# Kernel tuning notes

Measured on AMD Instinct MI355X. Metric: run time of the kernel, lower is better.

The kernel has to match this reference:

```python
import jax, jax.numpy as jnp
import numpy as np

V, D, L, H, T_BLK, DFF = 50257, 768, 12, 12, 1024, 4096
DK = D // H
LN_EPS = 1e-5


def setup_inputs() -> dict:
    key = jax.random.key(0)
    ks = jax.random.split(key, 16)
    s = 0.02
    inp = {
        "idx": jax.random.randint(ks[0], (2, 1024), 0, V),
        "tok_emb": jax.random.normal(ks[1], (V, D), jnp.float32) * s,
        "pos_emb": jax.random.normal(ks[2], (1, T_BLK, D), jnp.float32) * s,
        "ln1_w": jnp.ones((L, D), jnp.float32),
        "ln1_b": jnp.zeros((L, D), jnp.float32),
        "qkv_w": jax.random.normal(ks[3], (L, 3 * D, D), jnp.float32) * s,
        "qkv_b": jnp.zeros((L, 3 * D), jnp.float32),
        "proj_w": jax.random.normal(ks[4], (L, D, D), jnp.float32) * s,
        "proj_b": jnp.zeros((L, D), jnp.float32),
        "ln2_w": jnp.ones((L, D), jnp.float32),
        "ln2_b": jnp.zeros((L, D), jnp.float32),
        "ff1_w": jax.random.normal(ks[5], (L, DFF, D), jnp.float32) * s,
        "ff1_b": jnp.zeros((L, DFF), jnp.float32),
        "ff2_w": jax.random.normal(ks[6], (L, D, DFF), jnp.float32) * s,
        "ff2_b": jnp.zeros((L, D), jnp.float32),
        "lnf_w": jnp.ones((D,), jnp.float32),
        "lnf_b": jnp.zeros((D,), jnp.float32),
        "head_w": jax.random.normal(ks[7], (V, D), jnp.float32) * s,
    }
    return inp


def _layernorm(x, w, b):
    mu = jnp.mean(x, axis=-1, keepdims=True)
    var = jnp.var(x, axis=-1, keepdims=True)
    return (x - mu) * jax.lax.rsqrt(var + LN_EPS) * w + b


def _gpt_forward(idx, tok_emb, pos_emb, ln1_w, ln1_b, qkv_w, qkv_b, proj_w, proj_b,
                 ln2_w, ln2_b, ff1_w, ff1_b, ff2_w, ff2_b, lnf_w, lnf_b, head_w):
    B, T = idx.shape
    x = tok_emb[idx] + pos_emb[:, :T, :]  # [B,T,D]
    mask = jnp.tril(jnp.ones((T, T), bool))  # causal
    scale = 1.0 / np.sqrt(DK)

    def step(x, p):
        l1w, l1b, qw, qb, pw, pb, l2w, l2b, f1w, f1b, f2w, f2b = p
        h = _layernorm(x, l1w, l1b)
        qkv = h @ qw.T + qb  # [B,T,3D]
        q, k, v = jnp.split(qkv, 3, axis=-1)
        q = q.reshape(B, T, H, DK).transpose(0, 2, 1, 3)  # [B,H,T,DK]
        k = k.reshape(B, T, H, DK).transpose(0, 2, 1, 3)
        v = v.reshape(B, T, H, DK).transpose(0, 2, 1, 3)
        att = jnp.einsum('bhtd,bhsd->bhts', q, k) * scale
        att = jnp.where(mask, att, -jnp.inf)
        att = jax.nn.softmax(att, axis=-1)
        y = jnp.einsum('bhts,bhsd->bhtd', att, v)
        y = y.transpose(0, 2, 1, 3).reshape(B, T, D)
        x = x + y @ pw.T + pb
        h2 = _layernorm(x, l2w, l2b)
        ff = jax.nn.gelu(h2 @ f1w.T + f1b, approximate=False) @ f2w.T + f2b
        return x + ff, None

    params = (ln1_w, ln1_b, qkv_w, qkv_b, proj_w, proj_b,
              ln2_w, ln2_b, ff1_w, ff1_b, ff2_w, ff2_b)
    x, _ = jax.lax.scan(step, x, params)
    x = _layernorm(x, lnf_w, lnf_b)
    return x @ head_w.T  # [B,T,V] logits


def reference(idx, tok_emb, pos_emb, ln1_w, ln1_b, qkv_w, qkv_b, proj_w, proj_b,
              ln2_w, ln2_b, ff1_w, ff1_b, ff2_w, ff2_b, lnf_w, lnf_b, head_w):
    return _gpt_forward(idx, tok_emb, pos_emb, ln1_w, ln1_b, qkv_w, qkv_b, proj_w,
                        proj_b, ln2_w, ln2_b, ff1_w, ff1_b, ff2_w, ff2_b,
                        lnf_w, lnf_b, head_w)
```

## Files before the change

### kernel.cpp

```cpp
#include <hip/hip_runtime.h>
#include <hip/hip_bf16.h>
#include <math.h>

#define Dm 768
#define Tt 1024
#define Bb 2
#define Hh 12
#define DFF 4096
#define Ll 12
#define Vv 50257
#define ROWS (Bb*Tt)
#define LN_EPS 1e-5f

typedef unsigned int uint;
typedef unsigned short ushort;
typedef float f32x4 __attribute__((ext_vector_type(4)));
typedef short bf16x8 __attribute__((ext_vector_type(8)));
typedef ushort us8 __attribute__((ext_vector_type(8)));

__device__ __forceinline__ ushort f2bf(float f) {
  uint u = __builtin_bit_cast(uint, f);
  u += 0x7FFFu + ((u >> 16) & 1u);
  return (ushort)(u >> 16);
}

#define GLL(gp, lp)                                                          \
  __builtin_amdgcn_global_load_lds(                                          \
      (const __attribute__((address_space(1))) uint*)(gp),                   \
      (__attribute__((address_space(3))) uint*)(lp), 16, 0, 0)

__global__ __launch_bounds__(256) void embed_ln(
    const int* __restrict__ idx, const float* __restrict__ tok,
    const float* __restrict__ pos, const float* __restrict__ w,
    const float* __restrict__ b, float* __restrict__ x,
    ushort* __restrict__ out) {
  const int row = blockIdx.x;
  const int t = row & (Tt - 1);
  const int tid = threadIdx.x;
  const float* tsrc = tok + (size_t)idx[row] * Dm;
  const float* psrc = pos + (size_t)t * Dm;
  float v[3];
  float sum = 0.f, sq = 0.f;
#pragma unroll
  for (int i = 0; i < 3; i++) {
    const int d = tid + i * 256;
    v[i] = tsrc[d] + psrc[d];
    x[(size_t)row * Dm + d] = v[i];
    sum += v[i]; sq += v[i] * v[i];
  }
#pragma unroll
  for (int off = 32; off > 0; off >>= 1) {
    sum += __shfl_xor(sum, off);
    sq  += __shfl_xor(sq, off);
  }
  __shared__ float red[8];
  const int wid = tid >> 6, lane = tid & 63;
  if (lane == 0) { red[wid] = sum; red[wid + 4] = sq; }
  __syncthreads();
  sum = red[0] + red[1] + red[2] + red[3];
  sq  = red[4] + red[5] + red[6] + red[7];
  const float mu = sum * (1.f / Dm);
  const float var = sq * (1.f / Dm) - mu * mu;
  const float rstd = rsqrtf(var + LN_EPS);
  ushort* dst = out + (size_t)row * Dm;
#pragma unroll
  for (int i = 0; i < 3; i++) {
    const int d = tid + i * 256;
    dst[d] = f2bf((v[i] - mu) * rstd * w[d] + b[d]);
  }
}

__global__ __launch_bounds__(256) void red_ln(
    const float* __restrict__ part, int nsk, const float* __restrict__ bias,
    float* __restrict__ x, const float* __restrict__ w,
    const float* __restrict__ b, ushort* __restrict__ out) {
  const int row = blockIdx.x;
  const int tid = threadIdx.x;
  float v[3];
  float sum = 0.f, sq = 0.f;
#pragma unroll
  for (int i = 0; i < 3; i++) {
    const int d = tid + i * 256;
    const size_t off = (size_t)row * Dm + d;
    float s = x[off] + bias[d];
    for (int k = 0; k < nsk; k++) s += part[(size_t)k * ROWS * Dm + off];
    x[off] = s;
    v[i] = s;
    sum += s; sq += s * s;
  }
#pragma unroll
  for (int off = 32; off > 0; off >>= 1) {
    sum += __shfl_xor(sum, off);
    sq  += __shfl_xor(sq, off);
  }
  __shared__ float red[8];
  const int wid = tid >> 6, lane = tid & 63;
  if (lane == 0) { red[wid] = sum; red[wid + 4] = sq; }
  __syncthreads();
  sum = red[0] + red[1] + red[2] + red[3];
  sq  = red[4] + red[5] + red[6] + red[7];
  const float mu = sum * (1.f / Dm);
  const float var = sq * (1.f / Dm) - mu * mu;
  const float rstd = rsqrtf(var + LN_EPS);
  ushort* dst = out + (size_t)row * Dm;
#pragma unroll
  for (int i = 0; i < 3; i++) {
    const int d = tid + i * 256;
    dst[d] = f2bf((v[i] - mu) * rstd * w[d] + b[d]);
  }
}

__global__ __launch_bounds__(256) void convert_w(
    const float* __restrict__ s, ushort* __restrict__ d, int n4) {
  const int stride = gridDim.x * 256;
  for (int i = blockIdx.x * 256 + threadIdx.x; i < n4; i += stride) {
    const float4 v = ((const float4*)s)[i];
    ushort4 o;
    o.x = f2bf(v.x); o.y = f2bf(v.y); o.z = f2bf(v.z); o.w = f2bf(v.w);
    ((ushort4*)d)[i] = o;
  }
}

#define EPI_QKV 0
#define EPI_PART 1
#define EPI_BIAS_GELU 2
#define EPI_NONE 3

template <int EPI>
__global__ __launch_bounds__(256) void gemm_mfma(
    const ushort* __restrict__ A, const ushort* __restrict__ B,
    const float* __restrict__ bias, void* __restrict__ Cv,
    void* __restrict__ Cv2, int Kloop, int Kstr, int Nloc, int ldC) {
  __shared__ char lds[32768];
  const int tid = threadIdx.x;
  const int l = tid & 63;
  const int wid = __builtin_amdgcn_readfirstlane(tid >> 6);
  const int wr = wid >> 1, wc = wid & 1;
  const int m0 = blockIdx.y * 128;
  const int n0 = blockIdx.x * 128;
  const int z = (EPI == EPI_PART) ? blockIdx.z : 0;
  if (EPI == EPI_PART) { A += (size_t)z * Kloop; B += (size_t)z * Kloop; }

  const int cperm = (((l & 3) ^ ((l >> 3) & 3)) * 8);
  const ushort* gA = A + (size_t)(m0 + wid * 32 + (l >> 2)) * Kstr + cperm;
  int rB = n0 + wid * 32 + (l >> 2);
  rB = min(rB, Nloc - 1);
  const ushort* gB = B + (size_t)rB * Kstr + cperm;

  const int rdSw = (l & 15) * 64 + (((l >> 4) ^ ((l >> 1) & 3)) * 16);
  const int aRd = wr * 4096 + rdSw;
  const int bRd = 8192 + wc * 4096 + rdSw;

  f32x4 acc[4][4] = {};
  const int nt = Kloop / 32;

  {
    const int lb = wid * 2048;
    GLL(gA, lds + lb);          GLL(gA + 16 * Kstr, lds + lb + 1024);
    GLL(gB, lds + 8192 + lb);   GLL(gB + 16 * Kstr, lds + 8192 + lb + 1024);
  }

  for (int t = 0; t < nt; ++t) {
    __syncthreads();
    if (t + 1 < nt) {
      const int base = ((t + 1) & 1) * 16384;
      const int lb = base + wid * 2048;
      const ushort* a = gA + (t + 1) * 32;
      const ushort* b = gB + (t + 1) * 32;
      GLL(a, lds + lb);         GLL(a + 16 * Kstr, lds + lb + 1024);
      GLL(b, lds + 8192 + lb);  GLL(b + 16 * Kstr, lds + 8192 + lb + 1024);
    }
    const int base = (t & 1) * 16384;
    bf16x8 av[4], bv[4];
#pragma unroll
    for (int i = 0; i < 4; ++i) {
      av[i] = *(const bf16x8*)(lds + base + aRd + i * 1024);
      bv[i] = *(const bf16x8*)(lds + base + bRd + i * 1024);
    }
#pragma unroll
    for (int i = 0; i < 4; ++i)
#pragma unroll
      for (int j = 0; j < 4; ++j)
        acc[i][j] = __builtin_amdgcn_mfma_f32_16x16x32_bf16(
            av[i], bv[j], acc[i][j], 0, 0, 0);
  }

#pragma unroll
  for (int fm = 0; fm < 4; ++fm) {
    const int row0 = m0 + wr * 64 + fm * 16 + (l >> 4) * 4;
#pragma unroll
    for (int fn = 0; fn < 4; ++fn) {
      const int col = n0 + wc * 64 + fn * 16 + (l & 15);
      if (col >= Nloc) continue;
      float bi = 0.f;
      if (EPI == EPI_QKV || EPI == EPI_BIAS_GELU) bi = bias[col];
      if (EPI == EPI_QKV && col >= 2 * Dm) {
        const int hh = (col - 2 * Dm) >> 6, dd = col & 63;
        const int bI = row0 >> 10, t0 = row0 & (Tt - 1);
        ushort4 o4;
        o4.x = f2bf(acc[fm][fn][0] + bi);
        o4.y = f2bf(acc[fm][fn][1] + bi);
        o4.z = f2bf(acc[fm][fn][2] + bi);
        o4.w = f2bf(acc[fm][fn][3] + bi);
        *(ushort4*)((ushort*)Cv2 +
                    ((size_t)((bI * Hh + hh) * 64 + dd)) * Tt + t0) = o4;
        continue;
      }
#pragma unroll
      for (int r = 0; r < 4; ++r) {
        float v = acc[fm][fn][r] + bi;
        const size_t off = (size_t)(row0 + r) * ldC + col;
        if (EPI == EPI_BIAS_GELU) {
          v = 0.5f * v * (1.f + erff(v * 0.70710678118654752f));
          ((ushort*)Cv)[off] = f2bf(v);
        } else if (EPI == EPI_QKV) {
          ((ushort*)Cv)[off] = f2bf(v);
        } else if (EPI == EPI_PART) {
          ((float*)Cv)[(size_t)z * ROWS * ldC + off] = v;
        } else {
          ((float*)Cv)[off] = v;
        }
      }
    }
  }
}

__global__ __launch_bounds__(128) void attn_mfma(
    const ushort* __restrict__ qkv, const ushort* __restrict__ vTg,
    ushort* __restrict__ y) {
  __shared__ char lds[36864];
  const int tid = threadIdx.x;
  const int l = tid & 63;
  const int w = tid >> 6;
  const int s = l & 15, g = l >> 4;
  const int bq = blockIdx.x, h = blockIdx.y, b = blockIdx.z;
  const int bh = b * Hh + h;

  const int qrow = bq * 32 + w * 16 + s;
  const ushort* qp = qkv + (size_t)(b * Tt + qrow) * 2304 + h * 64 + g * 8;
  const bf16x8 aq0 = *(const bf16x8*)qp;
  const bf16x8 aq1 = *(const bf16x8*)(qp + 32);

  size_t gofs[8];
#pragma unroll
  for (int i = 0; i < 8; i++) {
    const int c = tid + i * 128;
    if (i < 4) {
      const int kr = c >> 3;
      gofs[i] = (size_t)(b * Tt + kr) * 2304 + Dm + h * 64 + ((c & 7) ^ (kr & 7)) * 8;
    } else {
      const int cv = c - 512;
      const int vr = cv >> 3;
      gofs[i] = (size_t)(bh * 64 + vr) * Tt + ((cv & 7) ^ (vr & 7)) * 8;
    }
  }

#define ASTAGE(kt, base)                                                     \
  do {                                                                       \
    _Pragma("unroll")                                                        \
    for (int i = 0; i < 8; i++) {                                            \
      const ushort* p = (i < 4) ? (qkv + gofs[i] + (size_t)(kt) * 147456)    \
                                : (vTg + gofs[i] + (kt) * 64);               \
      GLL(p, lds + (base) + tid * 16 + i * 2048);                            \
    }                                                                        \
  } while (0)

  f32x4 oc[4] = {};
  float mrun[4], lrun[4];
#pragma unroll
  for (int r = 0; r < 4; r++) { mrun[r] = -INFINITY; lrun[r] = 0.f; }

  const int pB = 32768 + w * 2048;
  const int kSw = (s & 7);
  const int nkt = (bq >> 1) + 1;

  ASTAGE(0, 0);
  for (int kt = 0; kt < nkt; ++kt) {
    __syncthreads();
    if (kt + 1 < nkt) ASTAGE(kt + 1, ((kt + 1) & 1) * 16384);
    const int cur = (kt & 1) * 16384;

    f32x4 sc[4];
#pragma unroll
    for (int jn = 0; jn < 4; jn++) {
      const int krow = cur + (jn * 16 + s) * 128;
      const bf16x8 bk0 = *(const bf16x8*)(lds + krow + ((g ^ kSw) * 16));
      const bf16x8 bk1 = *(const bf16x8*)(lds + krow + (((4 + g) ^ kSw) * 16));
      f32x4 z = {};
      z = __builtin_amdgcn_mfma_f32_16x16x32_bf16(aq0, bk0, z, 0, 0, 0);
      z = __builtin_amdgcn_mfma_f32_16x16x32_bf16(aq1, bk1, z, 0, 0, 0);
      sc[jn] = z;
    }

    float cr[4];
    const bool diag = (kt == nkt - 1);
#pragma unroll
    for (int r = 0; r < 4; r++) {
      const int rowg = bq * 32 + w * 16 + g * 4 + r;
      float v[4];
#pragma unroll
      for (int jn = 0; jn < 4; jn++) {
        v[jn] = sc[jn][r] * 0.125f;
        if (diag && (kt * 64 + jn * 16 + s) > rowg) v[jn] = -INFINITY;
      }
      float mx = fmaxf(fmaxf(v[0], v[1]), fmaxf(v[2], v[3]));
      mx = fmaxf(mx, __shfl_xor(mx, 1));
      mx = fmaxf(mx, __shfl_xor(mx, 2));
      mx = fmaxf(mx, __shfl_xor(mx, 4));
      mx = fmaxf(mx, __shfl_xor(mx, 8));
      const float mnew = fmaxf(mrun[r], mx);
      const float corr = __expf(mrun[r] - mnew);
      mrun[r] = mnew;
      float ps = 0.f;
#pragma unroll
      for (int jn = 0; jn < 4; jn++) {
        const float p = __expf(v[jn] - mnew);
        ps += p;
        *(ushort*)(lds + pB + (g * 4 + r) * 128 +
                   (((2 * jn + (s >> 3)) ^ g) * 16) + (s & 7) * 2) = f2bf(p);
      }
      ps += __shfl_xor(ps, 1);
      ps += __shfl_xor(ps, 2);
      ps += __shfl_xor(ps, 4);
      ps += __shfl_xor(ps, 8);
      lrun[r] = lrun[r] * corr + ps;
      cr[r] = corr;
    }

    const float c01 = (s & 1) ? cr[1] : cr[0];
    const float c23 = (s & 1) ? cr[3] : cr[2];
    const float csel = (s & 2) ? c23 : c01;
    const float ccol = __shfl(csel, ((s >> 2) << 4) | s);
#pragma unroll
    for (int fm = 0; fm < 4; fm++) {
      oc[fm][0] *= ccol; oc[fm][1] *= ccol;
      oc[fm][2] *= ccol; oc[fm][3] *= ccol;
    }

    const bf16x8 bp0 = *(const bf16x8*)(lds + pB + s * 128 + ((g ^ (s >> 2)) * 16));
    const bf16x8 bp1 = *(const bf16x8*)(lds + pB + s * 128 + (((4 + g) ^ (s >> 2)) * 16));
#pragma unroll
    for (int fm = 0; fm < 4; fm++) {
      const int vrow = cur + 8192 + (fm * 16 + s) * 128;
      const bf16x8 av0 = *(const bf16x8*)(lds + vrow + ((g ^ kSw) * 16));
      const bf16x8 av1 = *(const bf16x8*)(lds + vrow + (((4 + g) ^ kSw) * 16));
      oc[fm] = __builtin_amdgcn_mfma_f32_16x16x32_bf16(av0, bp0, oc[fm], 0, 0, 0);
      oc[fm] = __builtin_amdgcn_mfma_f32_16x16x32_bf16(av1, bp1, oc[fm], 0, 0, 0);
    }
  }

  float li[4];
#pragma unroll
  for (int r = 0; r < 4; r++) li[r] = 1.f / lrun[r];
  const float l01 = (s & 1) ? li[1] : li[0];
  const float l23 = (s & 1) ? li[3] : li[2];
  const float lsel = (s & 2) ? l23 : l01;
  const float lcol = __shfl(lsel, ((s >> 2) << 4) | s);
  ushort* yp = y + (size_t)(b * Tt + qrow) * Dm + h * 64;
#pragma unroll
  for (int fm = 0; fm < 4; fm++) {
    ushort4 o4;
    o4.x = f2bf(oc[fm][0] * lcol);
    o4.y = f2bf(oc[fm][1] * lcol);
    o4.z = f2bf(oc[fm][2] * lcol);
    o4.w = f2bf(oc[fm][3] * lcol);
    *(ushort4*)(yp + fm * 16 + g * 4) = o4;
  }
}

extern "C" void kernel_launch(void* const* d_in, const int* in_sizes, int n_in,
                              void* d_out, int out_size, void* d_ws, size_t ws_size,
                              hipStream_t stream) {
  const int* idx = (const int*)d_in[0];
  const float* tok = (const float*)d_in[1];
  const float* pos = (const float*)d_in[2];
  const float* ln1w = (const float*)d_in[3];
  const float* ln1b = (const float*)d_in[4];
  const float* qkvw = (const float*)d_in[5];
  const float* qkvb = (const float*)d_in[6];
  const float* projw = (const float*)d_in[7];
  const float* projb = (const float*)d_in[8];
  const float* ln2w = (const float*)d_in[9];
  const float* ln2b = (const float*)d_in[10];
  const float* ff1w = (const float*)d_in[11];
  const float* ff1b = (const float*)d_in[12];
  const float* ff2w = (const float*)d_in[13];
  const float* ff2b = (const float*)d_in[14];
  const float* lnfw = (const float*)d_in[15];
  const float* lnfb = (const float*)d_in[16];
  const float* headw = (const float*)d_in[17];
  float* out = (float*)d_out;

  char* ws = (char*)d_ws;
  ushort* h    = (ushort*)ws;
  float*  x    = (float*)(ws + 3145728);
  ushort* y    = (ushort*)(ws + 9437184);
  ushort* qkv  = (ushort*)(ws + 12582912);
  ushort* vTg  = (ushort*)(ws + 22020096);
  ushort* ff   = (ushort*)(ws + 25165824);
  ushort* wb   = (ushort*)(ws + 41943040);
  float* projPart = (float*)(ws + 12582912);
  float* ff2Part  = (float*)(ws + 9437184);

  const size_t oPROJ = (size_t)Ll * 3 * Dm * Dm;
  const size_t oFF1  = oPROJ + (size_t)Ll * Dm * Dm;
  const size_t oFF2  = oFF1 + (size_t)Ll * DFF * Dm;
  const size_t oHEAD = oFF2 + (size_t)Ll * Dm * DFF;

  convert_w<<<2048, 256, 0, stream>>>(qkvw, wb, (int)(oPROJ / 4));
  convert_w<<<2048, 256, 0, stream>>>(projw, wb + oPROJ, (int)((oFF1 - oPROJ) / 4));
  convert_w<<<2048, 256, 0, stream>>>(ff1w, wb + oFF1, (int)((oFF2 - oFF1) / 4));
  convert_w<<<2048, 256, 0, stream>>>(ff2w, wb + oFF2, (int)((oHEAD - oFF2) / 4));
  convert_w<<<2048, 256, 0, stream>>>(headw, wb + oHEAD, (int)((size_t)Vv * Dm / 4));

  embed_ln<<<ROWS, 256, 0, stream>>>(idx, tok, pos, ln1w, ln1b, x, h);

  for (int l = 0; l < Ll; l++) {
    gemm_mfma<EPI_QKV><<<dim3(18, 16), 256, 0, stream>>>(
        h, wb + (size_t)l * 3 * Dm * Dm, qkvb + l * 3 * Dm, qkv, vTg,
        Dm, Dm, 3 * Dm, 3 * Dm);
    attn_mfma<<<dim3(32, Hh, Bb), 128, 0, stream>>>(qkv, vTg, y);
    gemm_mfma<EPI_PART><<<dim3(6, 16, 2), 256, 0, stream>>>(
        y, wb + oPROJ + (size_t)l * Dm * Dm, nullptr, projPart, nullptr,
        Dm / 2, Dm, Dm, Dm);
    red_ln<<<ROWS, 256, 0, stream>>>(projPart, 2, projb + l * Dm, x,
                                     ln2w + l * Dm, ln2b + l * Dm, h);
    gemm_mfma<EPI_BIAS_GELU><<<dim3(32, 16), 256, 0, stream>>>(
        h, wb + oFF1 + (size_t)l * DFF * Dm, ff1b + l * DFF, ff, nullptr,
        Dm, Dm, DFF, DFF);
    gemm_mfma<EPI_PART><<<dim3(6, 16, 2), 256, 0, stream>>>(
        ff, wb + oFF2 + (size_t)l * Dm * DFF, nullptr, ff2Part, nullptr,
        DFF / 2, DFF, Dm, Dm);
    const float* nw = (l == Ll - 1) ? lnfw : ln1w + (l + 1) * Dm;
    const float* nb = (l == Ll - 1) ? lnfb : ln1b + (l + 1) * Dm;
    red_ln<<<ROWS, 256, 0, stream>>>(ff2Part, 2, ff2b + l * Dm, x, nw, nb, h);
  }

  gemm_mfma<EPI_NONE><<<dim3(393, 16), 256, 0, stream>>>(
      h, wb + oHEAD, nullptr, out, nullptr, Dm, Dm, Vv, Vv);
}
```

Baseline: 2.245 ms.

## Add dedicated 256x256-tile LM-head GEMM with 4-stage pipeline; raise MFMA priority in attention

Replaces the generic GEMM used for the vocabulary projection with a specialized kernel using 256x256 output tiles, 8 waves, a 4-buffer async global-to-LDS pipeline over K=768, a swizzled block ordering for L2 reuse, and s_setprio around MFMA bursts. The larger tile is meant to raise arithmetic intensity and reduce operand refetch on the largest GEMM in the forward pass. It also wraps the attention MFMA loops with s_setprio. The tile uses 128KB of LDS and many accumulators, which risks low occupancy, and the ragged last vocab panel relies on clamped loads.

New measurement: 2.225 ms. About the same (-0.9%).

```diff
diff --git a/kernel.cpp b/kernel.cpp
--- a/kernel.cpp
+++ b/kernel.cpp
@@ -225,6 +225,106 @@
   }
 }
 
+__global__ __launch_bounds__(512, 2) void gemm_head8(
+    const ushort* __restrict__ A, const ushort* __restrict__ B,
+    float* __restrict__ C) {
+  __shared__ char lds[131072];
+  const int tid = threadIdx.x;
+  const int l = tid & 63;
+  const int wid = __builtin_amdgcn_readfirstlane(tid >> 6);
+  const int wm = wid >> 2, wn = wid & 3;
+
+  const int bid = blockIdx.x;
+  const int swz = (bid & 7) * 197 + (bid >> 3);
+  const int pan = swz >> 3, mrw = swz & 7;
+  const int m0 = mrw * 256;
+  const int n0 = pan * 256;
+
+  const ushort* gA[2];
+  const ushort* gB[2];
+#pragma unroll
+  for (int j = 0; j < 2; j++) {
+    const int c = tid + j * 512;
+    const int r = c >> 2, kq = c & 3;
+    gA[j] = A + (size_t)(m0 + r) * Dm + ((kq ^ (r & 3)) * 8);
+    int rb = n0 + r;
+    rb = min(rb, Vv - 1);
+    gB[j] = B + (size_t)rb * Dm + ((kq ^ (r & 3)) * 8);
+  }
+
+#define HSTAGE(t)                                                            \
+  do {                                                                       \
+    char* _lb = lds + ((t) & 3) * 32768;                                     \
+    const int _o = (t) * 32;                                                 \
+    GLL(gA[0] + _o, _lb + tid * 16);                                         \
+    GLL(gA[1] + _o, _lb + 8192 + tid * 16);                                  \
+    GLL(gB[0] + _o, _lb + 16384 + tid * 16);                                 \
+    GLL(gB[1] + _o, _lb + 24576 + tid * 16);                                 \
+  } while (0)
+
+  f32x4 acc[8][4] = {};
+  const int s = l & 15, g = l >> 4;
+
+  int aOff[8], bOff[4];
+#pragma unroll
+  for (int fm = 0; fm < 8; fm++) {
+    const int r = wm * 128 + fm * 16 + s;
+    aOff[fm] = r * 64 + ((g ^ (r & 3)) * 16);
+  }
+#pragma unroll
+  for (int fn = 0; fn < 4; fn++) {
+    const int r = wn * 64 + fn * 16 + s;
+    bOff[fn] = 16384 + r * 64 + ((g ^ (r & 3)) * 16);
+  }
+
+  HSTAGE(0); HSTAGE(1); HSTAGE(2);
+  asm volatile("s_waitcnt vmcnt(8)" ::: "memory");
+  __builtin_amdgcn_s_barrier();
+  __builtin_amdgcn_sched_barrier(0);
+
+#define HITER(t, VC)                                                         \
+  {                                                                          \
+    if ((t) + 3 < 24) HSTAGE((t) + 3);                                       \
+    char* bb = lds + ((t) & 3) * 32768;                                      \
+    bf16x8 av[8], bv[4];                                                     \
+    _Pragma("unroll")                                                        \
+    for (int fm = 0; fm < 8; fm++) av[fm] = *(const bf16x8*)(bb + aOff[fm]); \
+    _Pragma("unroll")                                                        \
+    for (int fn = 0; fn < 4; fn++) bv[fn] = *(const bf16x8*)(bb + bOff[fn]); \
+    __builtin_amdgcn_s_setprio(1);                                           \
+    _Pragma("unroll")                                                        \
+    for (int fm = 0; fm < 8; fm++)                                           \
+      _Pragma("unroll")                                                      \
+      for (int fn = 0; fn < 4; fn++)                                         \
+        acc[fm][fn] = __builtin_amdgcn_mfma_f32_16x16x32_bf16(               \
+            av[fm], bv[fn], acc[fm][fn], 0, 0, 0);                           \
+    __builtin_amdgcn_s_setprio(0);                                           \
+    asm volatile("s_waitcnt lgkmcnt(0)" ::: "memory");                       \
+    asm volatile("s_waitcnt vmcnt(" #VC ")" ::: "memory");                   \
+    __builtin_amdgcn_s_barrier();                                            \
+    __builtin_amdgcn_sched_barrier(0);                                       \
+  }
+
+#pragma unroll 1
+  for (int t = 0; t <= 20; ++t) HITER(t, 8);
+  HITER(21, 4);
+  HITER(22, 0);
+  HITER(23, 0);
+
+#pragma unroll
+  for (int fm = 0; fm < 8; ++fm) {
+    const int row0 = m0 + wm * 128 + fm * 16 + g * 4;
+#pragma unroll
+    for (int fn = 0; fn < 4; ++fn) {
+      const int col = n0 + wn * 64 + fn * 16 + s;
+      if (col >= Vv) continue;
+#pragma unroll
+      for (int r = 0; r < 4; ++r)
+        C[(size_t)(row0 + r) * Vv + col] = acc[fm][fn][r];
+    }
+  }
+}
+
 __global__ __launch_bounds__(128) void attn_mfma(
     const ushort* __restrict__ qkv, const ushort* __restrict__ vTg,
     ushort* __restrict__ y) {
@@ -281,6 +381,7 @@
     const int cur = (kt & 1) * 16384;
 
     f32x4 sc[4];
+    __builtin_amdgcn_s_setprio(1);
 #pragma unroll
     for (int jn = 0; jn < 4; jn++) {
       const int krow = cur + (jn * 16 + s) * 128;
@@ -291,6 +392,7 @@
       z = __builtin_amdgcn_mfma_f32_16x16x32_bf16(aq1, bk1, z, 0, 0, 0);
       sc[jn] = z;
     }
+    __builtin_amdgcn_s_setprio(0);
 
     float cr[4];
     const bool diag = (kt == nkt - 1);
@@ -339,6 +441,7 @@
 
     const bf16x8 bp0 = *(const bf16x8*)(lds + pB + s * 128 + ((g ^ (s >> 2)) * 16));
     const bf16x8 bp1 = *(const bf16x8*)(lds + pB + s * 128 + (((4 + g) ^ (s >> 2)) * 16));
+    __builtin_amdgcn_s_setprio(1);
 #pragma unroll
     for (int fm = 0; fm < 4; fm++) {
       const int vrow = cur + 8192 + (fm * 16 + s) * 128;
@@ -347,6 +450,7 @@
       oc[fm] = __builtin_amdgcn_mfma_f32_16x16x32_bf16(av0, bp0, oc[fm], 0, 0, 0);
       oc[fm] = __builtin_amdgcn_mfma_f32_16x16x32_bf16(av1, bp1, oc[fm], 0, 0, 0);
     }
+    __builtin_amdgcn_s_setprio(0);
   }
 
   float li[4];
@@ -436,6 +540,5 @@
     red_ln<<<ROWS, 256, 0, stream>>>(ff2Part, 2, ff2b + l * Dm, x, nw, nb, h);
   }
 
-  gemm_mfma<EPI_NONE><<<dim3(393, 16), 256, 0, stream>>>(
-      h, wb + oHEAD, nullptr, out, nullptr, Dm, Dm, Vv, Vv);
-}
+  gemm_head8<<<1576, 512, 0, stream>>>(h, wb + oHEAD, out);
+}
```
